# Optimization experiments

Measured on AMD Instinct MI355X. Metric: run time of the kernel, lower is better.

The kernel has to match this reference:

```python
import jax, jax.numpy as jnp
import numpy as np

T = 4096      # tokens (batch*seq)
D = 1024      # hidden_size
F = 4096      # intermediate_size
E = 8         # num_local_experts


def setup_inputs() -> dict:
    key = jax.random.key(0)
    ks = jax.random.split(key, 6)
    scale_in = 1.0 / np.sqrt(D)
    scale_f = 1.0 / np.sqrt(F)
    return {
        "x": jax.random.normal(ks[0], (T, D), jnp.float32),
        "gate_w": jax.random.normal(ks[1], (E, D), jnp.float32) * scale_in,
        "gate_b": jnp.zeros((E,), jnp.float32),
        "w1": jax.random.normal(ks[2], (E, F, D), jnp.float32) * scale_in,
        "w3": jax.random.normal(ks[3], (E, F, D), jnp.float32) * scale_in,
        "w2": jax.random.normal(ks[4], (E, D, F), jnp.float32) * scale_f,
        "top_k": 2,
    }


def reference(x, gate_w, gate_b, w1, w3, w2, top_k):
    # --- routing: gate linear -> softmax -> top-k, renormalized ---
    logits = x @ gate_w.T + gate_b                     # [T, E]
    probs = jax.nn.softmax(logits, axis=-1)            # [T, E]
    topk_p, topk_i = jax.lax.top_k(probs, top_k)       # [T, k]
    topk_p = topk_p / jnp.sum(topk_p, axis=-1, keepdims=True)
    # dense combine weights [T, E]: zeros except selected experts
    cw = jnp.zeros((x.shape[0], gate_w.shape[0]), x.dtype)
    cw = cw.at[jnp.arange(x.shape[0])[:, None], topk_i].set(topk_p)
    # --- experts: SwiGLU FFN, computed densely per expert, masked combine ---
    h1 = jnp.einsum('td,efd->etf', x, w1)              # [E, T, F]
    h3 = jnp.einsum('td,efd->etf', x, w3)              # [E, T, F]
    act = jax.nn.silu(h1) * h3                         # [E, T, F]
    expert_out = jnp.einsum('etf,edf->etd', act, w2)   # [E, T, D]
    out = jnp.einsum('etd,te->td', expert_out, cw)     # [T, D]
    return out
```

## Files before the change

kernel.cpp:

```cpp
#include <hip/hip_runtime.h>
#include <hip/hip_bf16.h>

#define T_TOK 4096
#define DIM   1024
#define FDIM  4096
#define NEXP  8
#define BM    128
#define BN    128
#define BK    32
#define AM    256
#define AK    32

typedef __attribute__((ext_vector_type(8))) short bf16x8_t;
typedef __attribute__((ext_vector_type(4))) float f32x4_t;

#define GLD16(gp, lp) __builtin_amdgcn_global_load_lds( \
    (const __attribute__((address_space(1))) unsigned int*)(gp), \
    (__attribute__((address_space(3))) unsigned int*)(lp), 16, 0, 0)

__device__ __forceinline__ unsigned short f2bf(float f) {
    union { __hip_bfloat16 h; unsigned short u; } c;
    c.h = __float2bfloat16(f);
    return c.u;
}
__device__ __forceinline__ uint4 pack8(const float4& a, const float4& b) {
    union { unsigned short s[8]; uint4 v; } u;
    u.s[0] = f2bf(a.x); u.s[1] = f2bf(a.y); u.s[2] = f2bf(a.z); u.s[3] = f2bf(a.w);
    u.s[4] = f2bf(b.x); u.s[5] = f2bf(b.y); u.s[6] = f2bf(b.z); u.s[7] = f2bf(b.w);
    return u.v;
}

__global__ __launch_bounds__(256) void convert_kernel(
    const float* __restrict__ src, unsigned short* __restrict__ dst, int n8)
{
    int i = blockIdx.x * 256 + threadIdx.x;
    if (i < n8) {
        const float4* s = reinterpret_cast<const float4*>(src) + (size_t)i * 2;
        float4 a = s[0], b = s[1];
        reinterpret_cast<uint4*>(dst)[i] = pack8(a, b);
    }
}

__global__ __launch_bounds__(256) void gate_kernel(
    const float* __restrict__ x, const float* __restrict__ gw,
    const float* __restrict__ gb, int* __restrict__ cnt,
    int* __restrict__ toklist, float* __restrict__ wlist)
{
    const int lane = threadIdx.x & 63;
    const int wv   = threadIdx.x >> 6;
    const int t    = blockIdx.x * 4 + wv;
    const float* xr = x + (size_t)t * DIM;

    float4 xv[4];
#pragma unroll
    for (int c = 0; c < 4; ++c)
        xv[c] = *reinterpret_cast<const float4*>(xr + c * 256 + lane * 4);

    float logit[NEXP];
#pragma unroll
    for (int e = 0; e < NEXP; ++e) {
        const float* gr = gw + e * DIM;
        float s = 0.f;
#pragma unroll
        for (int c = 0; c < 4; ++c) {
            float4 g = *reinterpret_cast<const float4*>(gr + c * 256 + lane * 4);
            s += xv[c].x * g.x + xv[c].y * g.y + xv[c].z * g.z + xv[c].w * g.w;
        }
#pragma unroll
        for (int o = 32; o > 0; o >>= 1) s += __shfl_xor(s, o, 64);
        logit[e] = s + gb[e];
    }

    if (lane == 0) {
        int i1 = 0;
#pragma unroll
        for (int e = 1; e < NEXP; ++e) if (logit[e] > logit[i1]) i1 = e;
        int i2 = (i1 == 0) ? 1 : 0;
#pragma unroll
        for (int e = 0; e < NEXP; ++e)
            if (e != i1 && e != i2 && logit[e] > logit[i2]) i2 = e;
        float eb = expf(logit[i2] - logit[i1]);
        float wA = 1.f / (1.f + eb);
        float wB = eb / (1.f + eb);
        int p = atomicAdd(&cnt[i1], 1);
        toklist[i1 * T_TOK + p] = t; wlist[i1 * T_TOK + p] = wA;
        p = atomicAdd(&cnt[i2], 1);
        toklist[i2 * T_TOK + p] = t; wlist[i2 * T_TOK + p] = wB;
    }
}

__global__ void offsets_kernel(const int* __restrict__ cnt, int* __restrict__ offs)
{
    if (threadIdx.x == 0) {
        int o = 0;
#pragma unroll
        for (int e = 0; e < NEXP; ++e) {
            offs[e] = o;
            o += ((cnt[e] + AM - 1) / AM) * AM;
        }
    }
}


#define ASTEP(TC, AFC, AFN, PF, RDNEXT, VM)                                    \
  {                                                                            \
    const unsigned short* bufc_ = lds + ((TC) & 3) * 16384;                    \
    bf16x8_t b1a_ = *reinterpret_cast<const bf16x8_t*>(bufc_ + 8192  + wnn * 1024 + swz);       \
    bf16x8_t b1b_ = *reinterpret_cast<const bf16x8_t*>(bufc_ + 8192  + wnn * 1024 + 512 + swz); \
    bf16x8_t b3a_ = *reinterpret_cast<const bf16x8_t*>(bufc_ + 12288 + wnn * 1024 + swz);       \
    bf16x8_t b3b_ = *reinterpret_cast<const bf16x8_t*>(bufc_ + 12288 + wnn * 1024 + 512 + swz); \
    if (RDNEXT) {                                                              \
      const unsigned short* bufn_ = lds + (((TC) + 1) & 3) * 16384 + wm * 4096 + swz; \
      _Pragma("unroll")                                                        \
      for (int i_ = 0; i_ < 8; ++i_)                                           \
        AFN[i_] = *reinterpret_cast<const bf16x8_t*>(bufn_ + i_ * 512);        \
    }                                                                          \
    __builtin_amdgcn_sched_barrier(0);                                         \
    if (PF) {                                                                  \
      const int pb_ = ((TC) + 3) & 3;                                          \
      GLD16(Ag0 + ((TC) + 3) * AK, lds + pb_ * 16384 + wv * 512);              \
      GLD16(Ag1 + ((TC) + 3) * AK, lds + pb_ * 16384 + (wv + 8) * 512);        \
      GLD16(B1g + ((TC) + 3) * AK, lds + pb_ * 16384 + 8192 + wv * 512);       \
      GLD16(B3g + ((TC) + 3) * AK, lds + pb_ * 16384 + 12288 + wv * 512);      \
    }                                                                          \
    __builtin_amdgcn_s_setprio(1);                                             \
    _Pragma("unroll")                                                          \
    for (int i_ = 0; i_ < 8; ++i_) {                                           \
      acc1[i_][0] = __builtin_amdgcn_mfma_f32_16x16x32_bf16(AFC[i_], b1a_, acc1[i_][0], 0, 0, 0); \
      acc1[i_][1] = __builtin_amdgcn_mfma_f32_16x16x32_bf16(AFC[i_], b1b_, acc1[i_][1], 0, 0, 0); \
      acc3[i_][0] = __builtin_amdgcn_mfma_f32_16x16x32_bf16(AFC[i_], b3a_, acc3[i_][0], 0, 0, 0); \
      acc3[i_][1] = __builtin_amdgcn_mfma_f32_16x16x32_bf16(AFC[i_], b3b_, acc3[i_][1], 0, 0, 0); \
    }                                                                          \
    __builtin_amdgcn_s_setprio(0);                                             \
    asm volatile("s_waitcnt " VM ::: "memory");                                \
    __builtin_amdgcn_s_barrier();                                              \
  }

__global__ __launch_bounds__(512, 2) void stageA_kernel(
    const unsigned short* __restrict__ xb, const unsigned short* __restrict__ w1b,
    const unsigned short* __restrict__ w3b, const int* __restrict__ cnt,
    const int* __restrict__ offs, const int* __restrict__ toklist,
    const unsigned short* __restrict__ zbuf, unsigned short* __restrict__ act)
{
    const int e  = blockIdx.z;
    const int c  = cnt[e];
    const int mt = blockIdx.y;
    if (mt * AM >= c) return;
    const int nt = blockIdx.x;
    const int n0 = nt * 128;

    __shared__ __align__(16) unsigned short lds[4 * 16384];

    const int tid  = threadIdx.x;
    const int lane = tid & 63;
    const int wv   = tid >> 6;
    const int wm   = wv >> 2;
    const int wnn  = wv & 3;
    const int quad = lane >> 4;
    const int r    = lane & 15;

    const int swz = (r * 32 + quad * 8) ^ (((r >> 1) & 3) << 3);

    const int wr = (lane >> 2) & 15;
    const int wc = (((lane ^ (lane >> 3)) & 1) << 3) |
                   ((((lane >> 1) ^ (lane >> 4)) & 1) << 4);

    const int stRow = wv * 16 + wr;
    const int ar0 = mt * AM + stRow;
    const int ar1 = ar0 + 128;
    const unsigned short* Ag0 = (ar0 < c)
        ? xb + (size_t)toklist[e * T_TOK + ar0] * DIM + wc : zbuf + wc;
    const unsigned short* Ag1 = (ar1 < c)
        ? xb + (size_t)toklist[e * T_TOK + ar1] * DIM + wc : zbuf + wc;
    const unsigned short* B1g = w1b + ((size_t)e * FDIM + n0 + stRow) * DIM + wc;
    const unsigned short* B3g = w3b + ((size_t)e * FDIM + n0 + stRow) * DIM + wc;

    f32x4_t acc1[8][2], acc3[8][2];
#pragma unroll
    for (int i = 0; i < 8; ++i)
#pragma unroll
        for (int j = 0; j < 2; ++j) {
            acc1[i][j] = (f32x4_t){0.f, 0.f, 0.f, 0.f};
            acc3[i][j] = (f32x4_t){0.f, 0.f, 0.f, 0.f};
        }

#pragma unroll
    for (int t = 0; t < 3; ++t) {
        GLD16(Ag0 + t * AK, lds + t * 16384 + wv * 512);
        GLD16(Ag1 + t * AK, lds + t * 16384 + (wv + 8) * 512);
        GLD16(B1g + t * AK, lds + t * 16384 + 8192 + wv * 512);
        GLD16(B3g + t * AK, lds + t * 16384 + 12288 + wv * 512);
    }
    asm volatile("s_waitcnt vmcnt(4)" ::: "memory");
    __builtin_amdgcn_s_barrier();

    bf16x8_t afA[8], afB[8];
    {
        const unsigned short* b0 = lds + wm * 4096 + swz;
#pragma unroll
        for (int i = 0; i < 8; ++i)
            afA[i] = *reinterpret_cast<const bf16x8_t*>(b0 + i * 512);
    }

#pragma unroll 1
    for (int t = 0; t < 28; t += 2) {
        ASTEP(t,     afA, afB, 1, 1, "vmcnt(4)");
        ASTEP(t + 1, afB, afA, 1, 1, "vmcnt(4)");
    }
    ASTEP(28, afA, afB, 1, 1, "vmcnt(4)");
    ASTEP(29, afB, afA, 0, 1, "vmcnt(0)");
    ASTEP(30, afA, afB, 0, 1, "vmcnt(0)");
    ASTEP(31, afB, afA, 0, 0, "vmcnt(0)");

    const size_t slot0 = (size_t)offs[e] + (size_t)mt * AM;
    unsigned short* abase = act + (slot0 + wm * 128 + quad * 4) * (size_t)FDIM
                          + n0 + wnn * 32 + r;
#pragma unroll
    for (int i = 0; i < 8; ++i)
#pragma unroll
        for (int j = 0; j < 2; ++j)
#pragma unroll
            for (int rr = 0; rr < 4; ++rr) {
                float h1 = acc1[i][j][rr];
                float h3 = acc3[i][j][rr];
                float sw = h1 / (1.f + __expf(-h1)) * h3;
                abase[(size_t)(i * 16 + rr) * FDIM + j * 16] = f2bf(sw);
            }
}

__global__ __launch_bounds__(256, 3) void stageB_kernel(
    const unsigned short* __restrict__ act, const unsigned short* __restrict__ w2b,
    const int* __restrict__ cnt, const int* __restrict__ offs,
    const int* __restrict__ toklist, const float* __restrict__ wlist,
    float* __restrict__ out)
{
    const int e  = blockIdx.z & 7;
    const int ks = blockIdx.z >> 3;
    const int c  = cnt[e];
    const int mt = blockIdx.y;
    if (mt * BM >= c) return;
    const int nt = blockIdx.x;
    const size_t slot0 = (size_t)offs[e] + (size_t)mt * BM;
    const int n0 = nt * BN;
    const int kbase = ks * (FDIM / 2);

    __shared__ __align__(16) unsigned short As[BM * BK];
    __shared__ __align__(16) unsigned short Bs[BN * BK];

    const int tid  = threadIdx.x;
    const int lane = tid & 63;
    const int wv   = tid >> 6;
    const int wm   = (wv & 1) * 64;
    const int wn   = (wv >> 1) * 64;
    const int quad = lane >> 4;
    const int r    = lane & 15;

    const int dRow = wv * 32 + (lane >> 2);
    const unsigned short* Adma = act + (slot0 + dRow) * FDIM + kbase + (lane & 3) * 8;
    const unsigned short* Bdma = w2b + ((size_t)e * DIM + n0 + dRow) * FDIM + kbase + (lane & 3) * 8;
    const int lds0 = (wv * 32) * BK;
    const int lds1 = (wv * 32 + 16) * BK;

    f32x4_t acc[4][4];
#pragma unroll
    for (int i = 0; i < 4; ++i)
#pragma unroll
        for (int j = 0; j < 4; ++j) acc[i][j] = (f32x4_t){0.f, 0.f, 0.f, 0.f};

    for (int kd = 0; kd < FDIM / 2; kd += BK) {
        __syncthreads();
        GLD16(Adma + kd,             &As[lds0]);
        GLD16(Adma + kd + 16 * FDIM, &As[lds1]);
        GLD16(Bdma + kd,             &Bs[lds0]);
        GLD16(Bdma + kd + 16 * FDIM, &Bs[lds1]);
        __syncthreads();

        bf16x8_t af[4];
#pragma unroll
        for (int i = 0; i < 4; ++i)
            af[i] = *reinterpret_cast<const bf16x8_t*>(&As[(wm + i * 16 + r) * BK + quad * 8]);
#pragma unroll
        for (int j = 0; j < 4; ++j) {
            bf16x8_t bf = *reinterpret_cast<const bf16x8_t*>(&Bs[(wn + j * 16 + r) * BK + quad * 8]);
#pragma unroll
            for (int i = 0; i < 4; ++i)
                acc[i][j] = __builtin_amdgcn_mfma_f32_16x16x32_bf16(af[i], bf, acc[i][j], 0, 0, 0);
        }
    }

    const int row0 = mt * BM;
#pragma unroll
    for (int i = 0; i < 4; ++i)
#pragma unroll
        for (int rr = 0; rr < 4; ++rr) {
            int m = wm + i * 16 + quad * 4 + rr;
            int row = row0 + m;
            if (row < c) {
                int tok  = toklist[e * T_TOK + row];
                float wt = wlist[e * T_TOK + row];
                float* orow = out + (size_t)tok * DIM + n0;
#pragma unroll
                for (int j = 0; j < 4; ++j) {
                    int n = wn + j * 16 + r;
                    atomicAdd(&orow[n], wt * acc[i][j][rr]);
                }
            }
        }
}

extern "C" void kernel_launch(void* const* d_in, const int* in_sizes, int n_in,
                              void* d_out, int out_size, void* d_ws, size_t ws_size,
                              hipStream_t stream)
{
    (void)in_sizes; (void)n_in; (void)out_size; (void)ws_size;
    const float* x  = (const float*)d_in[0];
    const float* gw = (const float*)d_in[1];
    const float* gb = (const float*)d_in[2];
    const float* w1 = (const float*)d_in[3];
    const float* w3 = (const float*)d_in[4];
    const float* w2 = (const float*)d_in[5];
    float* out = (float*)d_out;

    char* ws = (char*)d_ws;
    unsigned short* xb   = (unsigned short*)ws;
    unsigned short* act  = (unsigned short*)(ws + 8388608);
    unsigned short* w1b  = (unsigned short*)(ws + 92274688);
    unsigned short* w3b  = (unsigned short*)(ws + 159383552);
    unsigned short* w2b  = (unsigned short*)(ws + 226492416);
    unsigned short* zbuf = (unsigned short*)(ws + 293601280);
    int*   cnt     = (int*)(ws + 293605376);
    int*   offs    = cnt + 64;
    int*   toklist = cnt + 128;
    float* wlist   = (float*)(cnt + 128 + NEXP * T_TOK);

    hipMemsetAsync(cnt, 0, 64, stream);
    hipMemsetAsync(zbuf, 0, 4096, stream);
    hipMemsetAsync(out, 0, (size_t)T_TOK * DIM * sizeof(float), stream);

    const int n8 = NEXP * FDIM * DIM / 8;
    convert_kernel<<<n8 / 256, 256, 0, stream>>>(w1, w1b, n8);
    convert_kernel<<<n8 / 256, 256, 0, stream>>>(w3, w3b, n8);
    convert_kernel<<<n8 / 256, 256, 0, stream>>>(w2, w2b, n8);
    convert_kernel<<<(T_TOK * DIM / 8) / 256, 256, 0, stream>>>(x, xb, T_TOK * DIM / 8);

    gate_kernel<<<T_TOK / 4, 256, 0, stream>>>(x, gw, gb, cnt, toklist, wlist);
    offsets_kernel<<<1, 64, 0, stream>>>(cnt, offs);
    stageA_kernel<<<dim3(FDIM / 128, T_TOK / AM, NEXP), 512, 0, stream>>>(
        xb, w1b, w3b, cnt, offs, toklist, zbuf, act);
    stageB_kernel<<<dim3(DIM / BN, T_TOK / BM, NEXP * 2), 256, 0, stream>>>(
        act, w2b, cnt, offs, toklist, wlist, out);
}
```

Before: 822.7 us.

## Rewrite down-projection as pipelined full-K GEMM with separate weighted combine kernel

Stage B now runs each expert's down-projection over the full F dimension, using 512 threads, a 4-buffer LDS ring filled by direct global-to-LDS loads, swizzled fragments and prioritized MFMA. It writes unweighted per-slot outputs to a scratch buffer instead of issuing split-K float atomics into the output. A new combine kernel gathers each token's two expert rows and applies the routing weights, so the output memset is no longer needed. The gate kernel now also records each token's expert, slot position and weight. This trades atomic traffic and split-K redundancy for an extra scratch write and read, and the scratch reuses the w1b region of the workspace.

```diff
diff --git a/kernel.cpp b/kernel.cpp
--- a/kernel.cpp
+++ b/kernel.cpp
@@ -6,8 +6,6 @@
 #define FDIM  4096
 #define NEXP  8
 #define BM    128
-#define BN    128
-#define BK    32
 #define AM    256
 #define AK    32
 
@@ -44,7 +42,8 @@
 __global__ __launch_bounds__(256) void gate_kernel(
     const float* __restrict__ x, const float* __restrict__ gw,
     const float* __restrict__ gb, int* __restrict__ cnt,
-    int* __restrict__ toklist, float* __restrict__ wlist)
+    int* __restrict__ toklist, int* __restrict__ tokexp,
+    int* __restrict__ tokpos, float* __restrict__ tokwt)
 {
     const int lane = threadIdx.x & 63;
     const int wv   = threadIdx.x >> 6;
@@ -83,9 +82,11 @@
         float wA = 1.f / (1.f + eb);
         float wB = eb / (1.f + eb);
         int p = atomicAdd(&cnt[i1], 1);
-        toklist[i1 * T_TOK + p] = t; wlist[i1 * T_TOK + p] = wA;
+        toklist[i1 * T_TOK + p] = t;
+        tokexp[2 * t] = i1; tokpos[2 * t] = p; tokwt[2 * t] = wA;
         p = atomicAdd(&cnt[i2], 1);
-        toklist[i2 * T_TOK + p] = t; wlist[i2 * T_TOK + p] = wB;
+        toklist[i2 * T_TOK + p] = t;
+        tokexp[2 * t + 1] = i2; tokpos[2 * t + 1] = p; tokwt[2 * t + 1] = wB;
     }
 }
 
@@ -100,7 +101,6 @@
         }
     }
 }
-
 
 #define ASTEP(TC, AFC, AFN, PF, RDNEXT, VM)                                    \
   {                                                                            \
@@ -160,7 +160,6 @@
     const int r    = lane & 15;
 
     const int swz = (r * 32 + quad * 8) ^ (((r >> 1) & 3) << 3);
-
     const int wr = (lane >> 2) & 15;
     const int wc = (((lane ^ (lane >> 3)) & 1) << 3) |
                    ((((lane >> 1) ^ (lane >> 4)) & 1) << 4);
@@ -228,84 +227,142 @@
             }
 }
 
-__global__ __launch_bounds__(256, 3) void stageB_kernel(
+
+#define BSTEP(TC, AFC, AFN, PF, RDNEXT, VM)                                    \
+  {                                                                            \
+    const unsigned short* bufc_ = ldsB + ((TC) & 3) * 12288;                   \
+    bf16x8_t b1a_ = *reinterpret_cast<const bf16x8_t*>(bufc_ + 4096 + wnn * 1024 + swz);       \
+    bf16x8_t b1b_ = *reinterpret_cast<const bf16x8_t*>(bufc_ + 4096 + wnn * 1024 + 512 + swz); \
+    bf16x8_t b3a_ = *reinterpret_cast<const bf16x8_t*>(bufc_ + 8192 + wnn * 1024 + swz);       \
+    bf16x8_t b3b_ = *reinterpret_cast<const bf16x8_t*>(bufc_ + 8192 + wnn * 1024 + 512 + swz); \
+    if (RDNEXT) {                                                              \
+      const unsigned short* bufn_ = ldsB + (((TC) + 1) & 3) * 12288 + wm * 2048 + swz; \
+      _Pragma("unroll")                                                        \
+      for (int i_ = 0; i_ < 4; ++i_)                                           \
+        AFN[i_] = *reinterpret_cast<const bf16x8_t*>(bufn_ + i_ * 512);        \
+    }                                                                          \
+    __builtin_amdgcn_sched_barrier(0);                                         \
+    if (PF) {                                                                  \
+      const int pb_ = ((TC) + 3) & 3;                                          \
+      GLD16(Adma  + ((TC) + 3) * AK, ldsB + pb_ * 12288 + wv * 512);           \
+      GLD16(B1dma + ((TC) + 3) * AK, ldsB + pb_ * 12288 + 4096 + wv * 512);    \
+      GLD16(B3dma + ((TC) + 3) * AK, ldsB + pb_ * 12288 + 8192 + wv * 512);    \
+    }                                                                          \
+    __builtin_amdgcn_s_setprio(1);                                             \
+    _Pragma("unroll")                                                          \
+    for (int i_ = 0; i_ < 4; ++i_) {                                           \
+      acc1[i_][0] = __builtin_amdgcn_mfma_f32_16x16x32_bf16(AFC[i_], b1a_, acc1[i_][0], 0, 0, 0); \
+      acc1[i_][1] = __builtin_amdgcn_mfma_f32_16x16x32_bf16(AFC[i_], b1b_, acc1[i_][1], 0, 0, 0); \
+      acc3[i_][0] = __builtin_amdgcn_mfma_f32_16x16x32_bf16(AFC[i_], b3a_, acc3[i_][0], 0, 0, 0); \
+      acc3[i_][1] = __builtin_amdgcn_mfma_f32_16x16x32_bf16(AFC[i_], b3b_, acc3[i_][1], 0, 0, 0); \
+    }                                                                          \
+    __builtin_amdgcn_s_setprio(0);                                             \
+    asm volatile("s_waitcnt " VM ::: "memory");                                \
+    __builtin_amdgcn_s_barrier();                                              \
+  }
+
+__global__ __launch_bounds__(512, 2) void stageB_kernel(
     const unsigned short* __restrict__ act, const unsigned short* __restrict__ w2b,
     const int* __restrict__ cnt, const int* __restrict__ offs,
-    const int* __restrict__ toklist, const float* __restrict__ wlist,
-    float* __restrict__ out)
-{
-    const int e  = blockIdx.z & 7;
-    const int ks = blockIdx.z >> 3;
+    float* __restrict__ Yp)
+{
+    const int e  = blockIdx.z;
     const int c  = cnt[e];
     const int mt = blockIdx.y;
     if (mt * BM >= c) return;
     const int nt = blockIdx.x;
+    const int n0 = nt * 128;
     const size_t slot0 = (size_t)offs[e] + (size_t)mt * BM;
-    const int n0 = nt * BN;
-    const int kbase = ks * (FDIM / 2);
-
-    __shared__ __align__(16) unsigned short As[BM * BK];
-    __shared__ __align__(16) unsigned short Bs[BN * BK];
+
+    __shared__ __align__(16) unsigned short ldsB[4 * 12288];
 
     const int tid  = threadIdx.x;
     const int lane = tid & 63;
     const int wv   = tid >> 6;
-    const int wm   = (wv & 1) * 64;
-    const int wn   = (wv >> 1) * 64;
+    const int wm   = wv >> 2;
+    const int wnn  = wv & 3;
     const int quad = lane >> 4;
     const int r    = lane & 15;
 
-    const int dRow = wv * 32 + (lane >> 2);
-    const unsigned short* Adma = act + (slot0 + dRow) * FDIM + kbase + (lane & 3) * 8;
-    const unsigned short* Bdma = w2b + ((size_t)e * DIM + n0 + dRow) * FDIM + kbase + (lane & 3) * 8;
-    const int lds0 = (wv * 32) * BK;
-    const int lds1 = (wv * 32 + 16) * BK;
-
-    f32x4_t acc[4][4];
+    const int swz = (r * 32 + quad * 8) ^ (((r >> 1) & 3) << 3);
+    const int wr = (lane >> 2) & 15;
+    const int wc = (((lane ^ (lane >> 3)) & 1) << 3) |
+                   ((((lane >> 1) ^ (lane >> 4)) & 1) << 4);
+
+    const int stRow = wv * 16 + wr;
+    const unsigned short* Adma  = act + (slot0 + stRow) * (size_t)FDIM + wc;
+    const unsigned short* B1dma = w2b + ((size_t)e * DIM + n0 + stRow) * FDIM + wc;
+    const unsigned short* B3dma = w2b + ((size_t)e * DIM + n0 + 512 + stRow) * FDIM + wc;
+
+    f32x4_t acc1[4][2], acc3[4][2];
 #pragma unroll
     for (int i = 0; i < 4; ++i)
 #pragma unroll
-        for (int j = 0; j < 4; ++j) acc[i][j] = (f32x4_t){0.f, 0.f, 0.f, 0.f};
-
-    for (int kd = 0; kd < FDIM / 2; kd += BK) {
-        __syncthreads();
-        GLD16(Adma + kd,             &As[lds0]);
-        GLD16(Adma + kd + 16 * FDIM, &As[lds1]);
-        GLD16(Bdma + kd,             &Bs[lds0]);
-        GLD16(Bdma + kd + 16 * FDIM, &Bs[lds1]);
-        __syncthreads();
-
-        bf16x8_t af[4];
+        for (int j = 0; j < 2; ++j) {
+            acc1[i][j] = (f32x4_t){0.f, 0.f, 0.f, 0.f};
+            acc3[i][j] = (f32x4_t){0.f, 0.f, 0.f, 0.f};
+        }
+
+#pragma unroll
+    for (int t = 0; t < 3; ++t) {
+        GLD16(Adma  + t * AK, ldsB + t * 12288 + wv * 512);
+        GLD16(B1dma + t * AK, ldsB + t * 12288 + 4096 + wv * 512);
+        GLD16(B3dma + t * AK, ldsB + t * 12288 + 8192 + wv * 512);
+    }
+    asm volatile("s_waitcnt vmcnt(3)" ::: "memory");
+    __builtin_amdgcn_s_barrier();
+
+    bf16x8_t afA[4], afB[4];
+    {
+        const unsigned short* b0 = ldsB + wm * 2048 + swz;
 #pragma unroll
         for (int i = 0; i < 4; ++i)
-            af[i] = *reinterpret_cast<const bf16x8_t*>(&As[(wm + i * 16 + r) * BK + quad * 8]);
-#pragma unroll
-        for (int j = 0; j < 4; ++j) {
-            bf16x8_t bf = *reinterpret_cast<const bf16x8_t*>(&Bs[(wn + j * 16 + r) * BK + quad * 8]);
-#pragma unroll
-            for (int i = 0; i < 4; ++i)
-                acc[i][j] = __builtin_amdgcn_mfma_f32_16x16x32_bf16(af[i], bf, acc[i][j], 0, 0, 0);
-        }
-    }
-
-    const int row0 = mt * BM;
+            afA[i] = *reinterpret_cast<const bf16x8_t*>(b0 + i * 512);
+    }
+
+#pragma unroll 1
+    for (int t = 0; t < 124; t += 2) {
+        BSTEP(t,     afA, afB, 1, 1, "vmcnt(3)");
+        BSTEP(t + 1, afB, afA, 1, 1, "vmcnt(3)");
+    }
+    BSTEP(124, afA, afB, 1, 1, "vmcnt(3)");
+    BSTEP(125, afB, afA, 0, 1, "vmcnt(0)");
+    BSTEP(126, afA, afB, 0, 1, "vmcnt(0)");
+    BSTEP(127, afB, afA, 0, 0, "vmcnt(0)");
+
+    float* ybase = Yp + (slot0 + wm * 64 + quad * 4) * (size_t)DIM
+                 + n0 + wnn * 32 + r;
 #pragma unroll
     for (int i = 0; i < 4; ++i)
 #pragma unroll
-        for (int rr = 0; rr < 4; ++rr) {
-            int m = wm + i * 16 + quad * 4 + rr;
-            int row = row0 + m;
-            if (row < c) {
-                int tok  = toklist[e * T_TOK + row];
-                float wt = wlist[e * T_TOK + row];
-                float* orow = out + (size_t)tok * DIM + n0;
-#pragma unroll
-                for (int j = 0; j < 4; ++j) {
-                    int n = wn + j * 16 + r;
-                    atomicAdd(&orow[n], wt * acc[i][j][rr]);
-                }
+        for (int j = 0; j < 2; ++j)
+#pragma unroll
+            for (int rr = 0; rr < 4; ++rr) {
+                ybase[(size_t)(i * 16 + rr) * DIM + j * 16]       = acc1[i][j][rr];
+                ybase[(size_t)(i * 16 + rr) * DIM + j * 16 + 512] = acc3[i][j][rr];
             }
-        }
+}
+
+__global__ __launch_bounds__(256) void combine_kernel(
+    const float* __restrict__ Yp, const int* __restrict__ offs,
+    const int* __restrict__ tokexp, const int* __restrict__ tokpos,
+    const float* __restrict__ tokwt, float* __restrict__ out)
+{
+    int i = blockIdx.x * 256 + threadIdx.x;
+    int t  = i >> 8;
+    int d4 = i & 255;
+    int e0 = tokexp[2 * t],     e1 = tokexp[2 * t + 1];
+    int s0 = offs[e0] + tokpos[2 * t];
+    int s1 = offs[e1] + tokpos[2 * t + 1];
+    float w0 = tokwt[2 * t], w1 = tokwt[2 * t + 1];
+    float4 a = reinterpret_cast<const float4*>(Yp)[(size_t)s0 * 256 + d4];
+    float4 b = reinterpret_cast<const float4*>(Yp)[(size_t)s1 * 256 + d4];
+    float4 o;
+    o.x = w0 * a.x + w1 * b.x;
+    o.y = w0 * a.y + w1 * b.y;
+    o.z = w0 * a.z + w1 * b.z;
+    o.w = w0 * a.w + w1 * b.w;
+    reinterpret_cast<float4*>(out)[i] = o;
 }
 
 extern "C" void kernel_launch(void* const* d_in, const int* in_sizes, int n_in,
@@ -328,14 +385,16 @@
     unsigned short* w3b  = (unsigned short*)(ws + 159383552);
     unsigned short* w2b  = (unsigned short*)(ws + 226492416);
     unsigned short* zbuf = (unsigned short*)(ws + 293601280);
+    float* Yp = (float*)(ws + 92274688);
     int*   cnt     = (int*)(ws + 293605376);
     int*   offs    = cnt + 64;
     int*   toklist = cnt + 128;
-    float* wlist   = (float*)(cnt + 128 + NEXP * T_TOK);
+    int*   tokexp  = toklist + NEXP * T_TOK;
+    int*   tokpos  = tokexp + 2 * T_TOK;
+    float* tokwt   = (float*)(tokpos + 2 * T_TOK);
 
     hipMemsetAsync(cnt, 0, 64, stream);
     hipMemsetAsync(zbuf, 0, 4096, stream);
-    hipMemsetAsync(out, 0, (size_t)T_TOK * DIM * sizeof(float), stream);
 
     const int n8 = NEXP * FDIM * DIM / 8;
     convert_kernel<<<n8 / 256, 256, 0, stream>>>(w1, w1b, n8);
@@ -343,10 +402,13 @@
     convert_kernel<<<n8 / 256, 256, 0, stream>>>(w2, w2b, n8);
     convert_kernel<<<(T_TOK * DIM / 8) / 256, 256, 0, stream>>>(x, xb, T_TOK * DIM / 8);
 
-    gate_kernel<<<T_TOK / 4, 256, 0, stream>>>(x, gw, gb, cnt, toklist, wlist);
+    gate_kernel<<<T_TOK / 4, 256, 0, stream>>>(x, gw, gb, cnt, toklist,
+                                               tokexp, tokpos, tokwt);
     offsets_kernel<<<1, 64, 0, stream>>>(cnt, offs);
     stageA_kernel<<<dim3(FDIM / 128, T_TOK / AM, NEXP), 512, 0, stream>>>(
         xb, w1b, w3b, cnt, offs, toklist, zbuf, act);
-    stageB_kernel<<<dim3(DIM / BN, T_TOK / BM, NEXP * 2), 256, 0, stream>>>(
-        act, w2b, cnt, offs, toklist, wlist, out);
-}
+    stageB_kernel<<<dim3(DIM / 256, T_TOK / BM, NEXP), 512, 0, stream>>>(
+        act, w2b, cnt, offs, Yp);
+    combine_kernel<<<T_TOK * DIM / 4 / 256, 256, 0, stream>>>(
+        Yp, offs, tokexp, tokpos, tokwt, out);
+}
```

New measurement: 817.1 us. About the same (-0.7%).
